# Kernel optimization log

Hardware: AMD Instinct MI355X
Metric: run time of the kernel (lower is better)

Reference implementation:

```python
import jax, jax.numpy as jnp
import numpy as np

# static graph structure: B graphs, each with NPER nodes and DEG*NPER edges
B = 128        # graphs in batch
NPER = 400     # nodes per graph (fMRI atlas ROIs)
DEG = 16       # avg degree
EPG = NPER * DEG
E = B * EPG    # 819200 edges total
F_IN = 400     # num_features
H = 128        # hidden dim of GraphConv
C = 2          # num_classes
K1, K2, K3 = 320, 256, 205  # ceil(0.8*400), ceil(0.8*320), ceil(0.8*256)


def setup_inputs() -> dict:
    key = jax.random.key(0)
    ks = jax.random.split(key, 24)
    x = jax.random.normal(ks[0], (B * NPER, F_IN), dtype=jnp.float32)
    # edges constrained within each graph (PyG batched disjoint-union convention)
    src_l = jax.random.randint(ks[1], (B, EPG), 0, NPER)
    dst_l = jax.random.randint(ks[2], (B, EPG), 0, NPER)
    off = (jnp.arange(B, dtype=jnp.int32) * NPER)[:, None]
    edge_src = (src_l + off).reshape(-1).astype(jnp.int32)
    edge_dst = (dst_l + off).reshape(-1).astype(jnp.int32)
    batch = jnp.repeat(jnp.arange(B, dtype=jnp.int32), NPER)
    s = 0.05
    p = {
        'Wrel1': jax.random.normal(ks[3], (H, F_IN)) * s,
        'Wroot1': jax.random.normal(ks[4], (H, F_IN)) * s,
        'b1': jnp.zeros((H,), jnp.float32),
        'pw1': jax.random.normal(ks[5], (H,)) * s,
        'Wrel2': jax.random.normal(ks[6], (H, H)) * s,
        'Wroot2': jax.random.normal(ks[7], (H, H)) * s,
        'b2': jnp.zeros((H,), jnp.float32),
        'pw2': jax.random.normal(ks[8], (H,)) * s,
        'Wrel3': jax.random.normal(ks[9], (H, H)) * s,
        'Wroot3': jax.random.normal(ks[10], (H, H)) * s,
        'b3': jnp.zeros((H,), jnp.float32),
        'pw3': jax.random.normal(ks[11], (H,)) * s,
        'W1': jax.random.normal(ks[12], (128, 256)) * s,
        'bl1': jnp.zeros((128,), jnp.float32),
        'W2': jax.random.normal(ks[13], (64, 128)) * s,
        'bl2': jnp.zeros((64,), jnp.float32),
        'W3': jax.random.normal(ks[14], (C, 64)) * s,
        'bl3': jnp.zeros((C,), jnp.float32),
    }
    return dict(x=x, edge_src=edge_src, edge_dst=edge_dst, batch=batch, **p)


def _graph_conv(x, src, dst, emask, Wrel, b, Wroot):
    # PyG GraphConv: lin_rel(sum_j x_j) + lin_root(x_i); masked edges contribute 0
    msg = x[src] * emask[:, None]
    agg = jax.ops.segment_sum(msg, dst, num_segments=x.shape[0])
    return agg @ Wrel.T + b + x @ Wroot.T


def _topk_pool(x, src, dst, emask, w, npg, k):
    # score = x.w / ||w||; keep top-k per graph; gate kept x by tanh(score)
    score = (x @ w) / (jnp.linalg.norm(w) + 1e-16)
    vals, idx = jax.lax.top_k(score.reshape(B, npg), k)      # [B,k]
    perm = (jnp.arange(B, dtype=jnp.int32)[:, None] * npg + idx).reshape(-1)
    xk = x[perm] * jnp.tanh(vals).reshape(-1)[:, None]
    new_id = jnp.full((B * npg,), -1, jnp.int32).at[perm].set(
        jnp.arange(B * k, dtype=jnp.int32))
    ns, nd = new_id[src], new_id[dst]
    keep = (ns >= 0) & (nd >= 0)
    em2 = emask * keep.astype(emask.dtype)
    return xk, jnp.where(keep, ns, 0), jnp.where(keep, nd, 0), em2


def _readout(x, k):
    xr = x.reshape(B, k, H)
    return jnp.concatenate([xr.max(axis=1), xr.mean(axis=1)], axis=1)  # [B,256]


def reference(x, edge_src, edge_dst, batch,
              Wrel1, Wroot1, b1, pw1, Wrel2, Wroot2, b2, pw2,
              Wrel3, Wroot3, b3, pw3, W1, bl1, W2, bl2, W3, bl3):
    em = jnp.ones((E,), jnp.float32)
    h = jax.nn.relu(_graph_conv(x, edge_src, edge_dst, em, Wrel1, b1, Wroot1))
    h, s, d, em = _topk_pool(h, edge_src, edge_dst, em, pw1, NPER, K1)
    x1 = _readout(h, K1)
    h = jax.nn.relu(_graph_conv(h, s, d, em, Wrel2, b2, Wroot2))
    h, s, d, em = _topk_pool(h, s, d, em, pw2, K1, K2)
    x2 = _readout(h, K2)
    h = jax.nn.relu(_graph_conv(h, s, d, em, Wrel3, b3, Wroot3))
    h, s, d, em = _topk_pool(h, s, d, em, pw3, K2, K3)
    x3 = _readout(h, K3)
    z = x1 + x2 + x3
    z = jax.nn.relu(z @ W1.T + bl1)  # dropout is identity in eval mode
    z = jax.nn.relu(z @ W2.T + bl2)
    return jax.nn.log_softmax(z @ W3.T + bl3, axis=-1)
```

## Files before the change

kernel.cpp:

```cpp
#include <hip/hip_runtime.h>
#include <math.h>

#define BATCH 128
#define NPER 400
#define EPG 6400
#define NEDGE 819200
#define F_IN 400
#define HD 128
#define K1 320
#define K2 256
#define K3 205

typedef __bf16 bf16x8 __attribute__((ext_vector_type(8)));
typedef float f32x4 __attribute__((ext_vector_type(4)));

__device__ __forceinline__ unsigned short f2bf(float f) {
    unsigned u = __builtin_bit_cast(unsigned, f);
    unsigned r = u + 0x7fffu + ((u >> 16) & 1u);
    return (unsigned short)(r >> 16);
}
__device__ __forceinline__ float bf2f(unsigned short s) {
    unsigned u = ((unsigned)s) << 16;
    return __builtin_bit_cast(float, u);
}

static constexpr size_t SZ_TREL = 51200ull * 128 * 4;
static constexpr size_t OFF_TREL = 0;
static constexpr size_t OFF_H    = OFF_TREL + SZ_TREL;
static constexpr size_t OFF_HP   = OFF_H + SZ_TREL;
static constexpr size_t OFF_SC   = OFF_HP + 40960ull * 128 * 4;
static constexpr size_t OFF_EPK  = OFF_SC + 51200ull * 4;
static constexpr size_t OFF_Z    = OFF_EPK + (size_t)NEDGE * 4 * 3;
static constexpr size_t OFF_COFF = OFF_Z + 128ull * 256 * 4;
static constexpr size_t OFF_CDEG = OFF_COFF + 51200ull * 4;
static constexpr size_t OFF_CSRC = OFF_CDEG + 51200ull * 4;
static constexpr size_t OFF_W1H  = OFF_CSRC + (size_t)NEDGE * 4;
static constexpr size_t OFF_W1L  = OFF_W1H + 16ull * 13 * 512 * 2;
static constexpr size_t OFF_W2H  = OFF_W1L + 16ull * 13 * 512 * 2;
static constexpr size_t OFF_W2L  = OFF_W2H + 16ull * 4 * 512 * 2;
static constexpr size_t OFF_W3H  = OFF_W2L + 16ull * 4 * 512 * 2;
static constexpr size_t OFF_W3L  = OFF_W3H + 16ull * 4 * 512 * 2;

__global__ __launch_bounds__(64) void prep_w_all(
    const float* __restrict__ Wrel1, const float* __restrict__ Wroot1,
    const float* __restrict__ Wrel2, const float* __restrict__ Wroot2,
    const float* __restrict__ Wrel3, const float* __restrict__ Wroot3,
    unsigned short* __restrict__ b1h, unsigned short* __restrict__ b1l,
    unsigned short* __restrict__ b2h, unsigned short* __restrict__ b2l,
    unsigned short* __restrict__ b3h, unsigned short* __restrict__ b3l) {
    const int layer = blockIdx.z;
    const int s = blockIdx.x;
    const int ntile = blockIdx.y;
    const int Ks = (layer == 0) ? 13 : 4;
    const int Kd = (layer == 0) ? F_IN : HD;
    if (s >= Ks) return;
    const float* Wrel  = (layer == 0) ? Wrel1  : (layer == 1) ? Wrel2  : Wrel3;
    const float* Wroot = (layer == 0) ? Wroot1 : (layer == 1) ? Wroot2 : Wroot3;
    unsigned short* bh = (layer == 0) ? b1h : (layer == 1) ? b2h : b3h;
    unsigned short* bl = (layer == 0) ? b1l : (layer == 1) ? b2l : b3l;
    const int t = threadIdx.x;
    const int rowin = t & 15, qd = t >> 4;
    const int n = ntile * 16 + rowin;
    const int k = s * 32 + qd * 8;
    const float* src = (n < 128) ? &Wrel[(n & 127) * Kd] : &Wroot[(n & 127) * Kd];
    unsigned short hv[8], lv[8];
#pragma unroll
    for (int e = 0; e < 8; e++) {
        float f = (k + e < Kd) ? src[k + e] : 0.f;
        unsigned short hi = f2bf(f);
        hv[e] = hi;
        lv[e] = f2bf(f - bf2f(hi));
    }
    size_t o = ((size_t)ntile * Ks + s) * 512 + (size_t)t * 8;
#pragma unroll
    for (int e = 0; e < 8; e++) { bh[o + e] = hv[e]; bl[o + e] = lv[e]; }
}

template <int Ks, int Kd>
__global__ __launch_bounds__(256, 3) void gemm_mfma(
    const float* __restrict__ A,
    const unsigned short* __restrict__ bh_p, const unsigned short* __restrict__ bl_p,
    float* __restrict__ t_rel, float* __restrict__ h) {
    __shared__ char Alds[2][8192];
    const int tid = threadIdx.x;
    const int lane = tid & 63;
    const int wv = tid >> 6;
    const int lm = lane & 15;
    const int qd = (lane >> 4) & 3;
    const int bpx = gridDim.x >> 3;
    const int lb = ((int)blockIdx.x & 7) * bpx + ((int)blockIdx.x >> 3);
    const int m0 = lb * 64;
    const int nt0 = wv * 4;

    const int srow = tid >> 2;
    const int sqd = tid & 3;
    const int woff = ((srow >> 4) << 10) + (sqd << 8) + ((srow & 15) << 4);
    const float* Arow = A + (size_t)(m0 + srow) * Kd + sqd * 8;

    f32x4 acc[4][4];
#pragma unroll
    for (int i = 0; i < 4; i++)
#pragma unroll
        for (int j = 0; j < 4; j++) acc[i][j] = (f32x4){0.f, 0.f, 0.f, 0.f};

    auto gload = [&](int s, float4& x0, float4& x1) {
        if (s * 32 + sqd * 8 < Kd) {
            const float* p = Arow + s * 32;
            x0 = *(const float4*)p;
            x1 = *(const float4*)(p + 4);
        } else {
            x0 = make_float4(0.f, 0.f, 0.f, 0.f);
            x1 = x0;
        }
    };
    auto cvwrite = [&](int buf, const float4& x0, const float4& x1) {
        float fe[8] = {x0.x, x0.y, x0.z, x0.w, x1.x, x1.y, x1.z, x1.w};
        bf16x8 hv, lv;
#pragma unroll
        for (int e = 0; e < 8; e++) {
            __bf16 hb = (__bf16)fe[e];
            hv[e] = hb;
            lv[e] = (__bf16)(fe[e] - (float)hb);
        }
        *(bf16x8*)(&Alds[buf][woff]) = hv;
        *(bf16x8*)(&Alds[buf][4096 + woff]) = lv;
    };

    float4 r0a, r0b, r1a, r1b, r2a, r2b;
    gload(0, r0a, r0b);
    if (Ks > 1) gload(1, r1a, r1b);
    if (Ks > 2) gload(2, r2a, r2b);
    cvwrite(0, r0a, r0b);
    asm volatile("s_waitcnt lgkmcnt(0)" ::: "memory");
    __builtin_amdgcn_s_barrier();
    asm volatile("" ::: "memory");

#pragma unroll
    for (int s = 0; s < Ks; ++s) {
        bf16x8 bhc[4], blc[4];
#pragma unroll
        for (int j = 0; j < 4; j++)
            bhc[j] = *(const bf16x8*)&bh_p[((size_t)(nt0 + j) * Ks + s) * 512 + lane * 8];
#pragma unroll
        for (int j = 0; j < 4; j++)
            blc[j] = *(const bf16x8*)&bl_p[((size_t)(nt0 + j) * Ks + s) * 512 + lane * 8];

        const char* Ab = &Alds[s & 1][0];
        bf16x8 ah[4], al[4];
#pragma unroll
        for (int i = 0; i < 4; i++) {
            ah[i] = *(const bf16x8*)(Ab + i * 1024 + lane * 16);
            al[i] = *(const bf16x8*)(Ab + 4096 + i * 1024 + lane * 16);
        }

        __builtin_amdgcn_s_setprio(1);
#pragma unroll
        for (int j = 0; j < 4; j++)
#pragma unroll
            for (int i = 0; i < 4; i++)
                acc[i][j] = __builtin_amdgcn_mfma_f32_16x16x32_bf16(
                    ah[i], bhc[j], acc[i][j], 0, 0, 0);
#pragma unroll
        for (int j = 0; j < 4; j++)
#pragma unroll
            for (int i = 0; i < 4; i++)
                acc[i][j] = __builtin_amdgcn_mfma_f32_16x16x32_bf16(
                    al[i], bhc[j], acc[i][j], 0, 0, 0);
#pragma unroll
        for (int j = 0; j < 4; j++)
#pragma unroll
            for (int i = 0; i < 4; i++)
                acc[i][j] = __builtin_amdgcn_mfma_f32_16x16x32_bf16(
                    ah[i], blc[j], acc[i][j], 0, 0, 0);
        __builtin_amdgcn_s_setprio(0);

        if (s + 1 < Ks) {
            const int p1 = (s + 1) % 3;
            if (p1 == 0)      cvwrite((s + 1) & 1, r0a, r0b);
            else if (p1 == 1) cvwrite((s + 1) & 1, r1a, r1b);
            else              cvwrite((s + 1) & 1, r2a, r2b);
        }
        if (s + 3 < Ks) {
            const int p3 = (s + 3) % 3;
            if (p3 == 0)      gload(s + 3, r0a, r0b);
            else if (p3 == 1) gload(s + 3, r1a, r1b);
            else              gload(s + 3, r2a, r2b);
        }

        asm volatile("s_waitcnt lgkmcnt(0)" ::: "memory");
        __builtin_amdgcn_s_barrier();
        asm volatile("" ::: "memory");
    }
    float* out = (wv < 2) ? t_rel : h;
    const int colbase = (wv & 1) * 64;
#pragma unroll
    for (int i = 0; i < 4; i++)
#pragma unroll
        for (int j = 0; j < 4; j++) {
            int row = m0 + i * 16 + qd * 4;
            int col = colbase + j * 16 + lm;
#pragma unroll
            for (int r = 0; r < 4; r++)
                out[(size_t)(row + r) * 128 + col] = acc[i][j][r];
        }
}

__global__ __launch_bounds__(1024) void csr_build0(
    const int* __restrict__ gsrc, const int* __restrict__ gdst,
    int* __restrict__ csr_off, int* __restrict__ csr_deg, int* __restrict__ csr_src) {
    __shared__ int cnt[NPER];
    __shared__ int cur[NPER];
    __shared__ int sscan[512];
    const int g = ((int)blockIdx.x & 7) * 16 + ((int)blockIdx.x >> 3);
    const int t = threadIdx.x;
    for (int i = t; i < NPER; i += 1024) cnt[i] = 0;
    __syncthreads();
    for (int e = t; e < EPG; e += 1024) {
        int dl = gdst[g * EPG + e] - g * NPER;
        atomicAdd(&cnt[dl], 1);
    }
    __syncthreads();
    if (t < 512) sscan[t] = (t < NPER) ? cnt[t] : 0;
    __syncthreads();
    for (int d = 1; d < 512; d <<= 1) {
        int v = 0;
        if (t < 512 && t >= d) v = sscan[t - d];
        __syncthreads();
        if (t < 512 && t >= d) sscan[t] += v;
        __syncthreads();
    }
    if (t < NPER) {
        int excl = (t == 0) ? 0 : sscan[t - 1];
        int st = g * EPG + excl;
        csr_off[g * NPER + t] = st;
        csr_deg[g * NPER + t] = cnt[t];
        cur[t] = st;
    }
    __syncthreads();
    for (int e = t; e < EPG; e += 1024) {
        int eg = g * EPG + e;
        int dl = gdst[eg] - g * NPER;
        int slot = atomicAdd(&cur[dl], 1);
        csr_src[slot] = gsrc[eg];
    }
}

__global__ __launch_bounds__(256) void agg_score(
    const float* __restrict__ t_rel,
    const int* __restrict__ csr_off, const int* __restrict__ csr_deg,
    const int* __restrict__ csr_src,
    const float* __restrict__ bias, const float* __restrict__ pw,
    float* __restrict__ h, float* __restrict__ sc, int npg) {
    const int xcd = blockIdx.x & 7;
    const int j = blockIdx.x >> 3;
    const int bpg = npg >> 3;
    const int graph = xcd * (BATCH / 8) + j / bpg;
    const int nblk = j - (j / bpg) * bpg;
    const int hw = threadIdx.x >> 5;
    const int lane = threadIdx.x & 31;
    const int wid = graph * npg + nblk * 8 + hw;

    const int start = csr_off[wid];
    const int deg = csr_deg[wid];
    const size_t fo = (size_t)lane * 4;
    f32x4 a = {0.f, 0.f, 0.f, 0.f}, b = a, c = a, d4 = a;
    int e = 0;
    for (; e + 4 <= deg; e += 4) {
        int s0 = csr_src[start + e];
        int s1 = csr_src[start + e + 1];
        int s2 = csr_src[start + e + 2];
        int s3 = csr_src[start + e + 3];
        f32x4 v0 = *(const f32x4*)&t_rel[(size_t)s0 * 128 + fo];
        f32x4 v1 = *(const f32x4*)&t_rel[(size_t)s1 * 128 + fo];
        f32x4 v2 = *(const f32x4*)&t_rel[(size_t)s2 * 128 + fo];
        f32x4 v3 = *(const f32x4*)&t_rel[(size_t)s3 * 128 + fo];
        a += v0; b += v1; c += v2; d4 += v3;
    }
    for (; e < deg; e++) {
        int s0 = csr_src[start + e];
        f32x4 v0 = *(const f32x4*)&t_rel[(size_t)s0 * 128 + fo];
        a += v0;
    }
    a += b + c + d4;

    f32x4 bb = *(const f32x4*)&bias[fo];
    size_t o = (size_t)wid * 128 + fo;
    f32x4 hv = *(const f32x4*)&h[o];
#pragma unroll
    for (int q = 0; q < 4; q++) hv[q] = fmaxf(hv[q] + a[q] + bb[q], 0.f);
    *(f32x4*)&h[o] = hv;
    f32x4 pp = *(const f32x4*)&pw[fo];
    float d = hv[0] * pp[0] + hv[1] * pp[1] + hv[2] * pp[2] + hv[3] * pp[3];
    float nr = pp[0] * pp[0] + pp[1] * pp[1] + pp[2] * pp[2] + pp[3] * pp[3];
#pragma unroll
    for (int off = 16; off; off >>= 1) {
        d += __shfl_down(d, off, 32);
        nr += __shfl_down(nr, off, 32);
    }
    if (lane == 0) sc[wid] = d / (sqrtf(nr) + 1e-16f);
}

__global__ __launch_bounds__(1024) void topk_pool(
    const float* __restrict__ sc, const float* __restrict__ h,
    float* __restrict__ hp, float* __restrict__ z,
    const int* __restrict__ gsrc, const int* __restrict__ gdst,
    int* __restrict__ epk,
    int* __restrict__ csr_off, int* __restrict__ csr_deg, int* __restrict__ csr_src,
    int npg, int k, int mode) {
    __shared__ float svals[NPER];
    __shared__ int si[512];
    __shared__ int nid[NPER];
    __shared__ float tgs[K1];
    __shared__ int packed[EPG];
    __shared__ int cnt[K1];
    __shared__ int cur[K1];
    __shared__ int sscan[512];
    __shared__ float pmx[8][128], psm[8][128];
    const int g = ((int)blockIdx.x & 7) * 16 + ((int)blockIdx.x >> 3);
    const int t = threadIdx.x;

    for (int i = t; i < npg; i += 1024) svals[i] = sc[g * npg + i];
    if (t < K1) cnt[t] = 0;
    __syncthreads();
    if (t < npg) {
        const float mine = svals[t];
        int r = 0;
        for (int j4 = 0; j4 < npg; j4 += 4) {
            float4 v = *(const float4*)&svals[j4];
            r += (v.x > mine) ? 1 : ((v.x == mine) & (j4 + 0 < t)) ? 1 : 0;
            r += (v.y > mine) ? 1 : ((v.y == mine) & (j4 + 1 < t)) ? 1 : 0;
            r += (v.z > mine) ? 1 : ((v.z == mine) & (j4 + 2 < t)) ? 1 : 0;
            r += (v.w > mine) ? 1 : ((v.w == mine) & (j4 + 3 < t)) ? 1 : 0;
        }
        nid[t] = (r < k) ? r : -1;
        if (r < k) {
            si[r] = t;
            tgs[r] = tanhf(mine);
        }
    }
    __syncthreads();

    {
        const int f = t & 127;
        const int jq = t >> 7;
        float mx = -INFINITY, sm = 0.f;
        for (int j = jq; j < k; j += 8) {
            float v = h[(size_t)(g * npg + si[j]) * 128 + f] * tgs[j];
            if (mode != 2) hp[(size_t)(g * k + j) * 128 + f] = v;
            mx = fmaxf(mx, v);
            sm += v;
        }
        pmx[jq][f] = mx; psm[jq][f] = sm;
        __syncthreads();
        if (t < 128) {
            mx = pmx[0][t]; sm = psm[0][t];
#pragma unroll
            for (int q = 1; q < 8; q++) {
                mx = fmaxf(mx, pmx[q][t]);
                sm += psm[q][t];
            }
            z[g * 256 + t] += mx;
            z[g * 256 + 128 + t] += sm / (float)k;
        }
    }
    if (mode == 2) return;

    for (int e = t; e < EPG; e += 1024) {
        int eg = g * EPG + e;
        int sl, dl, m;
        if (mode == 0) { sl = gsrc[eg] - g * NPER; dl = gdst[eg] - g * NPER; m = 1; }
        else           { int p = epk[eg]; sl = p & 1023; dl = (p >> 10) & 1023; m = p >> 20; }
        int ns = nid[sl], nd = nid[dl];
        int keep = (m && ns >= 0 && nd >= 0) ? 1 : 0;
        epk[eg] = keep ? (ns | (nd << 10) | (1 << 20)) : 0;
        packed[e] = keep ? (ns | (nd << 16)) : -1;
        if (keep) atomicAdd(&cnt[nd], 1);
    }
    __syncthreads();
    if (t < 512) sscan[t] = (t < k) ? cnt[t] : 0;
    __syncthreads();
    for (int d = 1; d < 512; d <<= 1) {
        int v = 0;
        if (t < 512 && t >= d) v = sscan[t - d];
        __syncthreads();
        if (t < 512 && t >= d) sscan[t] += v;
        __syncthreads();
    }
    if (t < k) {
        int excl = (t == 0) ? 0 : sscan[t - 1];
        int st = g * EPG + excl;
        csr_off[g * k + t] = st;
        csr_deg[g * k + t] = cnt[t];
        cur[t] = st;
    }
    __syncthreads();
    for (int e = t; e < EPG; e += 1024) {
        int p = packed[e];
        if (p >= 0) {
            int ns = p & 0xffff, nd = p >> 16;
            int slot = atomicAdd(&cur[nd], 1);
            csr_src[slot] = g * k + ns;
        }
    }
}

__global__ __launch_bounds__(256) void mlp_head(const float* __restrict__ z,
                                                const float* __restrict__ W1,
                                                const float* __restrict__ bl1,
                                                const float* __restrict__ W2,
                                                const float* __restrict__ bl2,
                                                const float* __restrict__ W3,
                                                const float* __restrict__ bl3,
                                                float* __restrict__ out) {
    __shared__ float zs[256], l1[128], l2[64];
    const int g = blockIdx.x, t = threadIdx.x;
    zs[t] = z[g * 256 + t];
    __syncthreads();
    {
        const int o = t >> 1, half = t & 1;
        const float* w = &W1[o * 256 + half * 128];
        const float* zp = &zs[half * 128];
        float s = 0.f;
        for (int i = 0; i < 128; i++) s += w[i] * zp[i];
        s += __shfl_down(s, 1, 64);
        if (half == 0) l1[o] = fmaxf(s + bl1[o], 0.f);
    }
    __syncthreads();
    {
        const int o = t >> 2, q = t & 3;
        const float* w = &W2[o * 128 + q * 32];
        const float* lp = &l1[q * 32];
        float s = 0.f;
        for (int i = 0; i < 32; i++) s += w[i] * lp[i];
        s += __shfl_down(s, 2, 64);
        s += __shfl_down(s, 1, 64);
        if (q == 0) l2[o] = fmaxf(s + bl2[o], 0.f);
    }
    __syncthreads();
    if (t < 64) {
        float pa = W3[t] * l2[t];
        float pb = W3[64 + t] * l2[t];
#pragma unroll
        for (int off = 32; off; off >>= 1) {
            pa += __shfl_down(pa, off, 64);
            pb += __shfl_down(pb, off, 64);
        }
        if (t == 0) {
            float A = pa + bl3[0], B = pb + bl3[1];
            float m = fmaxf(A, B);
            float lse = m + logf(expf(A - m) + expf(B - m));
            out[g * 2 + 0] = A - lse;
            out[g * 2 + 1] = B - lse;
        }
    }
}

extern "C" void kernel_launch(void* const* d_in, const int* in_sizes, int n_in,
                              void* d_out, int out_size, void* d_ws, size_t ws_size,
                              hipStream_t stream) {
    const float* x        = (const float*)d_in[0];
    const int*   edge_src = (const int*)d_in[1];
    const int*   edge_dst = (const int*)d_in[2];
    const float* Wrel1 = (const float*)d_in[4];
    const float* Wroot1= (const float*)d_in[5];
    const float* b1    = (const float*)d_in[6];
    const float* pw1   = (const float*)d_in[7];
    const float* Wrel2 = (const float*)d_in[8];
    const float* Wroot2= (const float*)d_in[9];
    const float* b2    = (const float*)d_in[10];
    const float* pw2   = (const float*)d_in[11];
    const float* Wrel3 = (const float*)d_in[12];
    const float* Wroot3= (const float*)d_in[13];
    const float* b3    = (const float*)d_in[14];
    const float* pw3   = (const float*)d_in[15];
    const float* W1    = (const float*)d_in[16];
    const float* bl1   = (const float*)d_in[17];
    const float* W2    = (const float*)d_in[18];
    const float* bl2   = (const float*)d_in[19];
    const float* W3    = (const float*)d_in[20];
    const float* bl3   = (const float*)d_in[21];

    char* ws = (char*)d_ws;
    float* t_rel = (float*)(ws + OFF_TREL);
    float* h     = (float*)(ws + OFF_H);
    float* hp    = (float*)(ws + OFF_HP);
    float* sc    = (float*)(ws + OFF_SC);
    int*   epk   = (int*)(ws + OFF_EPK);
    float* z     = (float*)(ws + OFF_Z);
    int*   coff  = (int*)(ws + OFF_COFF);
    int*   cdeg  = (int*)(ws + OFF_CDEG);
    int*   csrc  = (int*)(ws + OFF_CSRC);
    unsigned short* w1h = (unsigned short*)(ws + OFF_W1H);
    unsigned short* w1l = (unsigned short*)(ws + OFF_W1L);
    unsigned short* w2h = (unsigned short*)(ws + OFF_W2H);
    unsigned short* w2l = (unsigned short*)(ws + OFF_W2L);
    unsigned short* w3h = (unsigned short*)(ws + OFF_W3H);
    unsigned short* w3l = (unsigned short*)(ws + OFF_W3L);

    hipMemsetAsync(z, 0, 128ull * 256 * 4, stream);
    prep_w_all<<<dim3(13, 16, 3), 64, 0, stream>>>(
        Wrel1, Wroot1, Wrel2, Wroot2, Wrel3, Wroot3,
        w1h, w1l, w2h, w2l, w3h, w3l);
    csr_build0<<<BATCH, 1024, 0, stream>>>(edge_src, edge_dst, coff, cdeg, csrc);

    gemm_mfma<13, F_IN><<<800, 256, 0, stream>>>(x, w1h, w1l, t_rel, h);
    agg_score<<<51200 / 8, 256, 0, stream>>>(t_rel, coff, cdeg, csrc, b1, pw1,
                                             h, sc, NPER);
    topk_pool<<<BATCH, 1024, 0, stream>>>(sc, h, hp, z, edge_src, edge_dst,
                                          epk, coff, cdeg, csrc,
                                          NPER, K1, 0);

    gemm_mfma<4, HD><<<640, 256, 0, stream>>>(hp, w2h, w2l, t_rel, h);
    agg_score<<<40960 / 8, 256, 0, stream>>>(t_rel, coff, cdeg, csrc, b2, pw2,
                                             h, sc, K1);
    topk_pool<<<BATCH, 1024, 0, stream>>>(sc, h, hp, z, nullptr, nullptr,
                                          epk, coff, cdeg, csrc,
                                          K1, K2, 1);

    gemm_mfma<4, HD><<<512, 256, 0, stream>>>(hp, w3h, w3l, t_rel, h);
    agg_score<<<32768 / 8, 256, 0, stream>>>(t_rel, coff, cdeg, csrc, b3, pw3,
                                             h, sc, K2);
    topk_pool<<<BATCH, 1024, 0, stream>>>(sc, h, nullptr, z, nullptr, nullptr,
                                          epk, coff, cdeg, csrc,
                                          K2, K3, 2);

    mlp_head<<<BATCH, 256, 0, stream>>>(z, W1, bl1, W2, bl2, W3, bl3, (float*)d_out);
}
```

Before: 399.6 us.

## Fuse CSR build into first GEMM launch and MLP head into final pool

The standalone CSR-building kernel is folded into the first GEMM launch as 128 extra blocks that run concurrently with the GEMM tiles, with the scan rewritten for 256 threads. The separate MLP head kernel is merged into the last topk_pool launch, which now computes the final z in shared memory and runs the three dense layers in place. The pooled max/mean gather loop is also unrolled by four with independent accumulators to expose more memory-level parallelism. Together these remove two kernel launches and their serialization, at the cost of extra shared memory in the GEMM and pool kernels, which may lower occupancy.

Result: faster. 381.6 us (-4.5%).

```diff
diff --git a/kernel.cpp b/kernel.cpp
--- a/kernel.cpp
+++ b/kernel.cpp
@@ -76,18 +76,64 @@
     for (int e = 0; e < 8; e++) { bh[o + e] = hv[e]; bl[o + e] = lv[e]; }
 }
 
-template <int Ks, int Kd>
+template <int Ks, int Kd, bool FUSE>
 __global__ __launch_bounds__(256, 3) void gemm_mfma(
     const float* __restrict__ A,
     const unsigned short* __restrict__ bh_p, const unsigned short* __restrict__ bl_p,
-    float* __restrict__ t_rel, float* __restrict__ h) {
+    float* __restrict__ t_rel, float* __restrict__ h, int gemm_blocks,
+    const int* __restrict__ gsrc, const int* __restrict__ gdst,
+    int* __restrict__ csr_off, int* __restrict__ csr_deg, int* __restrict__ csr_src) {
+    if constexpr (FUSE) {
+        if ((int)blockIdx.x >= gemm_blocks) {
+            __shared__ int cnt[NPER];
+            __shared__ int cur[NPER];
+            __shared__ int sscan[512];
+            const int b = (int)blockIdx.x - gemm_blocks;
+            const int g = (b & 7) * 16 + (b >> 3);
+            const int t = threadIdx.x;
+            for (int i = t; i < NPER; i += 256) cnt[i] = 0;
+            __syncthreads();
+            for (int e = t; e < EPG; e += 256) {
+                int dl = gdst[g * EPG + e] - g * NPER;
+                atomicAdd(&cnt[dl], 1);
+            }
+            __syncthreads();
+            sscan[t] = (t < NPER) ? cnt[t] : 0;
+            sscan[t + 256] = (t + 256 < NPER) ? cnt[t + 256] : 0;
+            __syncthreads();
+            for (int d = 1; d < 256; d <<= 1) {
+                int va = (t >= d) ? sscan[t - d] : 0;
+                int vb = (t >= d) ? sscan[256 + t - d] : 0;
+                __syncthreads();
+                if (t >= d) { sscan[t] += va; sscan[256 + t] += vb; }
+                __syncthreads();
+            }
+            sscan[256 + t] += sscan[255];
+            __syncthreads();
+            for (int i = t; i < NPER; i += 256) {
+                int excl = (i == 0) ? 0 : sscan[i - 1];
+                int st = g * EPG + excl;
+                csr_off[g * NPER + i] = st;
+                csr_deg[g * NPER + i] = cnt[i];
+                cur[i] = st;
+            }
+            __syncthreads();
+            for (int e = t; e < EPG; e += 256) {
+                int eg = g * EPG + e;
+                int dl = gdst[eg] - g * NPER;
+                int slot = atomicAdd(&cur[dl], 1);
+                csr_src[slot] = gsrc[eg];
+            }
+            return;
+        }
+    }
     __shared__ char Alds[2][8192];
     const int tid = threadIdx.x;
     const int lane = tid & 63;
     const int wv = tid >> 6;
     const int lm = lane & 15;
     const int qd = (lane >> 4) & 3;
-    const int bpx = gridDim.x >> 3;
+    const int bpx = gemm_blocks >> 3;
     const int lb = ((int)blockIdx.x & 7) * bpx + ((int)blockIdx.x >> 3);
     const int m0 = lb * 64;
     const int nt0 = wv * 4;
@@ -203,46 +249,6 @@
             for (int r = 0; r < 4; r++)
                 out[(size_t)(row + r) * 128 + col] = acc[i][j][r];
         }
-}
-
-__global__ __launch_bounds__(1024) void csr_build0(
-    const int* __restrict__ gsrc, const int* __restrict__ gdst,
-    int* __restrict__ csr_off, int* __restrict__ csr_deg, int* __restrict__ csr_src) {
-    __shared__ int cnt[NPER];
-    __shared__ int cur[NPER];
-    __shared__ int sscan[512];
-    const int g = ((int)blockIdx.x & 7) * 16 + ((int)blockIdx.x >> 3);
-    const int t = threadIdx.x;
-    for (int i = t; i < NPER; i += 1024) cnt[i] = 0;
-    __syncthreads();
-    for (int e = t; e < EPG; e += 1024) {
-        int dl = gdst[g * EPG + e] - g * NPER;
-        atomicAdd(&cnt[dl], 1);
-    }
-    __syncthreads();
-    if (t < 512) sscan[t] = (t < NPER) ? cnt[t] : 0;
-    __syncthreads();
-    for (int d = 1; d < 512; d <<= 1) {
-        int v = 0;
-        if (t < 512 && t >= d) v = sscan[t - d];
-        __syncthreads();
-        if (t < 512 && t >= d) sscan[t] += v;
-        __syncthreads();
-    }
-    if (t < NPER) {
-        int excl = (t == 0) ? 0 : sscan[t - 1];
-        int st = g * EPG + excl;
-        csr_off[g * NPER + t] = st;
-        csr_deg[g * NPER + t] = cnt[t];
-        cur[t] = st;
-    }
-    __syncthreads();
-    for (int e = t; e < EPG; e += 1024) {
-        int eg = g * EPG + e;
-        int dl = gdst[eg] - g * NPER;
-        int slot = atomicAdd(&cur[dl], 1);
-        csr_src[slot] = gsrc[eg];
-    }
 }
 
 __global__ __launch_bounds__(256) void agg_score(
@@ -306,7 +312,11 @@
     const int* __restrict__ gsrc, const int* __restrict__ gdst,
     int* __restrict__ epk,
     int* __restrict__ csr_off, int* __restrict__ csr_deg, int* __restrict__ csr_src,
-    int npg, int k, int mode) {
+    int npg, int k, int mode,
+    const float* __restrict__ W1, const float* __restrict__ bl1,
+    const float* __restrict__ W2, const float* __restrict__ bl2,
+    const float* __restrict__ W3, const float* __restrict__ bl3,
+    float* __restrict__ outp) {
     __shared__ float svals[NPER];
     __shared__ int si[512];
     __shared__ int nid[NPER];
@@ -316,6 +326,7 @@
     __shared__ int cur[K1];
     __shared__ int sscan[512];
     __shared__ float pmx[8][128], psm[8][128];
+    __shared__ float zs[256], l1[128], l2[64];
     const int g = ((int)blockIdx.x & 7) * 16 + ((int)blockIdx.x >> 3);
     const int t = threadIdx.x;
 
@@ -343,27 +354,99 @@
     {
         const int f = t & 127;
         const int jq = t >> 7;
-        float mx = -INFINITY, sm = 0.f;
-        for (int j = jq; j < k; j += 8) {
+        float mx0 = -INFINITY, mx1 = -INFINITY, mx2 = -INFINITY, mx3 = -INFINITY;
+        float sm0 = 0.f, sm1 = 0.f, sm2 = 0.f, sm3 = 0.f;
+        int j = jq;
+        for (; j + 24 < k; j += 32) {
+            int i0 = si[j], i1 = si[j + 8], i2 = si[j + 16], i3 = si[j + 24];
+            float v0 = h[(size_t)(g * npg + i0) * 128 + f] * tgs[j];
+            float v1 = h[(size_t)(g * npg + i1) * 128 + f] * tgs[j + 8];
+            float v2 = h[(size_t)(g * npg + i2) * 128 + f] * tgs[j + 16];
+            float v3 = h[(size_t)(g * npg + i3) * 128 + f] * tgs[j + 24];
+            if (mode != 2) {
+                hp[(size_t)(g * k + j) * 128 + f] = v0;
+                hp[(size_t)(g * k + j + 8) * 128 + f] = v1;
+                hp[(size_t)(g * k + j + 16) * 128 + f] = v2;
+                hp[(size_t)(g * k + j + 24) * 128 + f] = v3;
+            }
+            mx0 = fmaxf(mx0, v0); sm0 += v0;
+            mx1 = fmaxf(mx1, v1); sm1 += v1;
+            mx2 = fmaxf(mx2, v2); sm2 += v2;
+            mx3 = fmaxf(mx3, v3); sm3 += v3;
+        }
+        for (; j < k; j += 8) {
             float v = h[(size_t)(g * npg + si[j]) * 128 + f] * tgs[j];
             if (mode != 2) hp[(size_t)(g * k + j) * 128 + f] = v;
-            mx = fmaxf(mx, v);
-            sm += v;
-        }
-        pmx[jq][f] = mx; psm[jq][f] = sm;
+            mx0 = fmaxf(mx0, v); sm0 += v;
+        }
+        pmx[jq][f] = fmaxf(fmaxf(mx0, mx1), fmaxf(mx2, mx3));
+        psm[jq][f] = (sm0 + sm1) + (sm2 + sm3);
         __syncthreads();
         if (t < 128) {
-            mx = pmx[0][t]; sm = psm[0][t];
+            float mx = pmx[0][t], sm = psm[0][t];
 #pragma unroll
             for (int q = 1; q < 8; q++) {
                 mx = fmaxf(mx, pmx[q][t]);
                 sm += psm[q][t];
             }
-            z[g * 256 + t] += mx;
-            z[g * 256 + 128 + t] += sm / (float)k;
-        }
-    }
-    if (mode == 2) return;
+            if (mode != 2) {
+                z[g * 256 + t] += mx;
+                z[g * 256 + 128 + t] += sm / (float)k;
+            } else {
+                zs[t] = z[g * 256 + t] + mx;
+                zs[128 + t] = z[g * 256 + 128 + t] + sm / (float)k;
+            }
+        }
+    }
+
+    if (mode == 2) {
+        __syncthreads();
+        {
+            const int o = t >> 3, oc = t & 7;
+            const float* w = &W1[o * 256 + oc * 32];
+            const float* zp = &zs[oc * 32];
+            float s = 0.f;
+#pragma unroll
+            for (int i = 0; i < 32; i++) s += w[i] * zp[i];
+            s += __shfl_down(s, 4, 8);
+            s += __shfl_down(s, 2, 8);
+            s += __shfl_down(s, 1, 8);
+            if (oc == 0) l1[o] = fmaxf(s + bl1[o], 0.f);
+        }
+        __syncthreads();
+        {
+            const int o = t >> 4, oc = t & 15;
+            const float* w = &W2[o * 128 + oc * 8];
+            const float* lp = &l1[oc * 8];
+            float s = 0.f;
+#pragma unroll
+            for (int i = 0; i < 8; i++) s += w[i] * lp[i];
+            s += __shfl_down(s, 8, 16);
+            s += __shfl_down(s, 4, 16);
+            s += __shfl_down(s, 2, 16);
+            s += __shfl_down(s, 1, 16);
+            if (oc == 0) l2[o] = fmaxf(s + bl2[o], 0.f);
+        }
+        __syncthreads();
+        if (t < 64) {
+            float pa = W3[t] * l2[t];
+            float pb = W3[64 + t] * l2[t];
+#pragma unroll
+            for (int off = 32; off; off >>= 1) {
+                pa += __shfl_down(pa, off, 64);
+                pb += __shfl_down(pb, off, 64);
+            }
+            if (t == 0) {
+                float A = pa + bl3[0], B = pb + bl3[1];
+                float m = fmaxf(A, B);
+                float lse = m + logf(expf(A - m) + expf(B - m));
+                outp[g * 2 + 0] = A - lse;
+                outp[g * 2 + 1] = B - lse;
+            }
+        }
+        return;
+    }
+    __syncthreads();
 
     for (int e = t; e < EPG; e += 1024) {
         int eg = g * EPG + e;
@@ -400,57 +483,6 @@
             int ns = p & 0xffff, nd = p >> 16;
             int slot = atomicAdd(&cur[nd], 1);
             csr_src[slot] = g * k + ns;
-        }
-    }
-}
-
-__global__ __launch_bounds__(256) void mlp_head(const float* __restrict__ z,
-                                                const float* __restrict__ W1,
-                                                const float* __restrict__ bl1,
-                                                const float* __restrict__ W2,
-                                                const float* __restrict__ bl2,
-                                                const float* __restrict__ W3,
-                                                const float* __restrict__ bl3,
-                                                float* __restrict__ out) {
-    __shared__ float zs[256], l1[128], l2[64];
-    const int g = blockIdx.x, t = threadIdx.x;
-    zs[t] = z[g * 256 + t];
-    __syncthreads();
-    {
-        const int o = t >> 1, half = t & 1;
-        const float* w = &W1[o * 256 + half * 128];
-        const float* zp = &zs[half * 128];
-        float s = 0.f;
-        for (int i = 0; i < 128; i++) s += w[i] * zp[i];
-        s += __shfl_down(s, 1, 64);
-        if (half == 0) l1[o] = fmaxf(s + bl1[o], 0.f);
-    }
-    __syncthreads();
-    {
-        const int o = t >> 2, q = t & 3;
-        const float* w = &W2[o * 128 + q * 32];
-        const float* lp = &l1[q * 32];
-        float s = 0.f;
-        for (int i = 0; i < 32; i++) s += w[i] * lp[i];
-        s += __shfl_down(s, 2, 64);
-        s += __shfl_down(s, 1, 64);
-        if (q == 0) l2[o] = fmaxf(s + bl2[o], 0.f);
-    }
-    __syncthreads();
-    if (t < 64) {
-        float pa = W3[t] * l2[t];
-        float pb = W3[64 + t] * l2[t];
-#pragma unroll
-        for (int off = 32; off; off >>= 1) {
-            pa += __shfl_down(pa, off, 64);
-            pb += __shfl_down(pb, off, 64);
-        }
-        if (t == 0) {
-            float A = pa + bl3[0], B = pb + bl3[1];
-            float m = fmaxf(A, B);
-            float lse = m + logf(expf(A - m) + expf(B - m));
-            out[g * 2 + 0] = A - lse;
-            out[g * 2 + 1] = B - lse;
         }
     }
 }
@@ -501,28 +533,34 @@
     prep_w_all<<<dim3(13, 16, 3), 64, 0, stream>>>(
         Wrel1, Wroot1, Wrel2, Wroot2, Wrel3, Wroot3,
         w1h, w1l, w2h, w2l, w3h, w3l);
-    csr_build0<<<BATCH, 1024, 0, stream>>>(edge_src, edge_dst, coff, cdeg, csrc);
-
-    gemm_mfma<13, F_IN><<<800, 256, 0, stream>>>(x, w1h, w1l, t_rel, h);
+
+    gemm_mfma<13, F_IN, true><<<800 + BATCH, 256, 0, stream>>>(
+        x, w1h, w1l, t_rel, h, 800, edge_src, edge_dst, coff, cdeg, csrc);
     agg_score<<<51200 / 8, 256, 0, stream>>>(t_rel, coff, cdeg, csrc, b1, pw1,
                                              h, sc, NPER);
     topk_pool<<<BATCH, 1024, 0, stream>>>(sc, h, hp, z, edge_src, edge_dst,
                                           epk, coff, cdeg, csrc,
-                                          NPER, K1, 0);
-
-    gemm_mfma<4, HD><<<640, 256, 0, stream>>>(hp, w2h, w2l, t_rel, h);
+                                          NPER, K1, 0,
+                                          nullptr, nullptr, nullptr, nullptr,
+                                          nullptr, nullptr, nullptr);
+
+    gemm_mfma<4, HD, false><<<640, 256, 0, stream>>>(
+        hp, w2h, w2l, t_rel, h, 640, nullptr, nullptr, nullptr, nullptr, nullptr);
     agg_score<<<40960 / 8, 256, 0, stream>>>(t_rel, coff, cdeg, csrc, b2, pw2,
                                              h, sc, K1);
     topk_pool<<<BATCH, 1024, 0, stream>>>(sc, h, hp, z, nullptr, nullptr,
                                           epk, coff, cdeg, csrc,
-                                          K1, K2, 1);
-
-    gemm_mfma<4, HD><<<512, 256, 0, stream>>>(hp, w3h, w3l, t_rel, h);
+                                          K1, K2, 1,
+                                          nullptr, nullptr, nullptr, nullptr,
+                                          nullptr, nullptr, nullptr);
+
+    gemm_mfma<4, HD, false><<<512, 256, 0, stream>>>(
+        hp, w3h, w3l, t_rel, h, 512, nullptr, nullptr, nullptr, nullptr, nullptr);
     agg_score<<<32768 / 8, 256, 0, stream>>>(t_rel, coff, cdeg, csrc, b3, pw3,
                                              h, sc, K2);
     topk_pool<<<BATCH, 1024, 0, stream>>>(sc, h, nullptr, z, nullptr, nullptr,
                                           epk, coff, cdeg, csrc,
-                                          K2, K3, 2);
-
-    mlp_head<<<BATCH, 256, 0, stream>>>(z, W1, bl1, W2, bl2, W3, bl3, (float*)d_out);
-}
+                                          K2, K3, 2,
+                                          W1, bl1, W2, bl2, W3, bl3,
+                                          (float*)d_out);
+}
```
